# Kernel optimization log

Measured on AMD Instinct MI355X. Metric: run time of the kernel, lower is better.

## Reference

```python
import jax, jax.numpy as jnp
import numpy as np

N_P, N_A, N_S = 100000, 150000, 1000
D_IN, N_HID, N_OUT = 256, 256, 64
E_PA, E_PS = 800000, 100000
HOP = 3


def spmm(row, col, val, h, n_rows):
    # sparse A (edge list) @ dense h : gather source rows, scale, scatter-add to dest rows
    return jax.ops.segment_sum(val[:, None] * h[col], row, num_segments=n_rows)


def setup_inputs() -> dict:
    key = jax.random.key(0)
    ks = jax.random.split(key, 30)
    inp = {}
    inp['x_P'] = jax.random.normal(ks[0], (N_P, D_IN), jnp.float32)
    inp['x_A'] = jax.random.normal(ks[1], (N_A, D_IN), jnp.float32)
    inp['x_S'] = jax.random.normal(ks[2], (N_S, D_IN), jnp.float32)
    inp['pa_row'] = jax.random.randint(ks[3], (E_PA,), 0, N_P, jnp.int32)
    inp['pa_col'] = jax.random.randint(ks[4], (E_PA,), 0, N_A, jnp.int32)
    inp['pa_val'] = jax.random.uniform(ks[5], (E_PA,), jnp.float32)
    inp['ps_row'] = jax.random.randint(ks[6], (E_PS,), 0, N_P, jnp.int32)
    inp['ps_col'] = jax.random.randint(ks[7], (E_PS,), 0, N_S, jnp.int32)
    inp['ps_val'] = jax.random.uniform(ks[8], (E_PS,), jnp.float32)
    inp['ap_row'] = jax.random.randint(ks[9], (E_PA,), 0, N_A, jnp.int32)
    inp['ap_col'] = jax.random.randint(ks[10], (E_PA,), 0, N_P, jnp.int32)
    inp['ap_val'] = jax.random.uniform(ks[11], (E_PA,), jnp.float32)
    inp['sp_row'] = jax.random.randint(ks[12], (E_PS,), 0, N_S, jnp.int32)
    inp['sp_col'] = jax.random.randint(ks[13], (E_PS,), 0, N_P, jnp.int32)
    inp['sp_val'] = jax.random.uniform(ks[14], (E_PS,), jnp.float32)
    inp['diag_PA'] = jax.random.uniform(ks[15], (N_P, 1), jnp.float32)
    inp['diag_PS'] = jax.random.uniform(ks[16], (N_P, 1), jnp.float32)
    inp['diag_AP'] = jax.random.uniform(ks[17], (N_A, 1), jnp.float32)
    inp['diag_SP'] = jax.random.uniform(ks[18], (N_S, 1), jnp.float32)
    s1 = 0.05
    inp['W1_P'] = jax.random.normal(ks[19], (D_IN, N_HID), jnp.float32) * s1
    inp['b1_P'] = jnp.zeros((N_HID,), jnp.float32)
    inp['W1_A'] = jax.random.normal(ks[20], (D_IN, N_HID), jnp.float32) * s1
    inp['b1_A'] = jnp.zeros((N_HID,), jnp.float32)
    inp['W1_S'] = jax.random.normal(ks[21], (D_IN, N_HID), jnp.float32) * s1
    inp['b1_S'] = jnp.zeros((N_HID,), jnp.float32)
    inp['W2'] = jax.random.normal(ks[22], (N_HID, N_OUT), jnp.float32) * s1
    inp['b2'] = jnp.zeros((N_OUT,), jnp.float32)
    return inp


def reference(x_P, x_A, x_S,
              pa_row, pa_col, pa_val,
              ps_row, ps_col, ps_val,
              ap_row, ap_col, ap_val,
              sp_row, sp_col, sp_val,
              diag_PA, diag_PS, diag_AP, diag_SP,
              W1_P, b1_P, W1_A, b1_A, W1_S, b1_S, W2, b2):
    # input projections (dropout is identity in eval mode)
    xP = jax.nn.relu(x_P @ W1_P + b1_P)
    xA = jax.nn.relu(x_A @ W1_A + b1_A)
    xS = jax.nn.relu(x_S @ W1_S + b1_S)
    hP, hA, hS = xP, xA, xS
    # hop loop; node types updated sequentially (P, A, S) as in the torch dict loop
    for _ in range(HOP):
        hP = 0.5 * ((spmm(pa_row, pa_col, pa_val, hA, N_P) + diag_PA * xP)
                    + (spmm(ps_row, ps_col, ps_val, hS, N_P) + diag_PS * xP))
        hA = spmm(ap_row, ap_col, ap_val, hP, N_A) + diag_AP * xA
        hS = spmm(sp_row, sp_col, sp_val, hP, N_S) + diag_SP * xS
    # target_node_type = 'P'
    return hP @ W2 + b2
```

## Files before the change

kernel.cpp:

```cpp
#include <hip/hip_runtime.h>
#include <hip/hip_bf16.h>


typedef __attribute__((ext_vector_type(8))) short bf16x8;
typedef __attribute__((ext_vector_type(4))) float f32x4;

__device__ inline unsigned short f2bf(float f) {
    unsigned u = __builtin_bit_cast(unsigned, f);
    u += 0x7FFFu + ((u >> 16) & 1u);
    return (unsigned short)(u >> 16);
}
__device__ inline float bflo(unsigned u) { return __builtin_bit_cast(float, u << 16); }
__device__ inline float bfhi(unsigned u) { return __builtin_bit_cast(float, u & 0xffff0000u); }

__device__ inline void bar_sync() {
    __builtin_amdgcn_sched_barrier(0);
    asm volatile("s_waitcnt lgkmcnt(0)" ::: "memory");
    __builtin_amdgcn_s_barrier();
    __builtin_amdgcn_sched_barrier(0);
}

__global__ void k_prep_count(const float* __restrict__ W1P, const float* __restrict__ W1A,
                             const float* __restrict__ W1S, const float* __restrict__ W2f,
                             unsigned short* __restrict__ out,
                             const int* __restrict__ pa, const int* __restrict__ ps,
                             const int* __restrict__ ap, const int* __restrict__ sp,
                             int* __restrict__ cnt, int nP, int nA, int ePA, int ePS) {
    int i = blockIdx.x * 256 + threadIdx.x;
    if (i < 3 * 65536) {
        int m = i >> 16;
        int r = i & 65535;
        int j = r & 7, l = (r >> 3) & 63, kk = (r >> 9) & 7, nt = (r >> 12) & 15;
        int col = nt * 16 + (l & 15);
        int k = kk * 32 + ((l >> 4) << 3) + j;
        const float* s = (m == 0) ? W1P : (m == 1) ? W1A : W1S;
        out[i] = f2bf(s[k * 256 + col]);
        return;
    } else if (i < 3 * 65536 + 16384) {
        int r = i - 3 * 65536;
        int j = r & 7, l = (r >> 3) & 63, kk = (r >> 9) & 7, nt = (r >> 12) & 3;
        int col = nt * 16 + (l & 15);
        int k = kk * 32 + ((l >> 4) << 3) + j;
        out[i] = f2bf(W2f[k * 64 + col]);
        return;
    }
    i -= 212992;
    int r, base;
    if (i < 0) return;
    if (i < ePA) { r = pa[i]; base = 0; }
    else if (i < ePA + ePS) { r = ps[i - ePA]; base = nP; }
    else if (i < 2 * ePA + ePS) { r = ap[i - ePA - ePS]; base = 2 * nP; }
    else if (i < 2 * ePA + 2 * ePS) { r = sp[i - 2 * ePA - ePS]; base = 2 * nP + nA; }
    else return;
    atomicAdd(&cnt[base + r], 1);
}

__global__ __launch_bounds__(256)
void k_proj_all(const float* __restrict__ xP, const float* __restrict__ xA,
                const float* __restrict__ xS, const unsigned short* __restrict__ Wpk,
                const float* __restrict__ b1P, const float* __restrict__ b1A,
                const float* __restrict__ b1S,
                unsigned short* __restrict__ yP, unsigned short* __restrict__ yA,
                unsigned short* __restrict__ yS, int nP, int nA, int nS) {
    __shared__ unsigned short xs[32 * 256];
    const int TP = (nP + 31) >> 5, TA = (nA + 31) >> 5, TS = (nS + 31) >> 5;
    const int TT = TP + TA + TS;
    const int tid = threadIdx.x, lane = tid & 63, w = tid >> 6;
    const int l15 = lane & 15, lhi = lane >> 4;
    const unsigned short* W2pk = Wpk + 3 * 65536;

    float4 xr[8];
    int t = blockIdx.x;
    if (t >= TT) return;

    {
        const float* x; int r0, nn;
        if (t < TP) { x = xP; r0 = t << 5; nn = nP; }
        else if (t < TP + TA) { x = xA; r0 = (t - TP) << 5; nn = nA; }
        else { x = xS; r0 = (t - TP - TA) << 5; nn = nS; }
        #pragma unroll
        for (int j = 0; j < 4; ++j) {
            int c = tid + j * 256;
            int row = c >> 5, col = (c & 31) << 3;
            int gr = r0 + row;
            float4 z = make_float4(0, 0, 0, 0);
            xr[2 * j] = z; xr[2 * j + 1] = z;
            if (gr < nn) {
                const float4* p = (const float4*)(x + (size_t)gr * 256 + col);
                xr[2 * j] = p[0]; xr[2 * j + 1] = p[1];
            }
        }
    }
    while (t < TT) {
        const unsigned short* W1; const float* b1; unsigned short* y; int r0, nn;
        if (t < TP) { r0 = t << 5; nn = nP; W1 = Wpk; b1 = b1P; y = yP; }
        else if (t < TP + TA) { r0 = (t - TP) << 5; nn = nA; W1 = Wpk + 65536; b1 = b1A; y = yA; }
        else { r0 = (t - TP - TA) << 5; nn = nS; W1 = Wpk + 2 * 65536; b1 = b1S; y = yS; }

        bar_sync();
        #pragma unroll
        for (int j = 0; j < 4; ++j) {
            int c = tid + j * 256;
            int row = c >> 5, col = (c & 31) << 3;
            float4 f0 = xr[2 * j], f1 = xr[2 * j + 1];
            bf16x8 v;
            v[0] = (short)f2bf(f0.x); v[1] = (short)f2bf(f0.y);
            v[2] = (short)f2bf(f0.z); v[3] = (short)f2bf(f0.w);
            v[4] = (short)f2bf(f1.x); v[5] = (short)f2bf(f1.y);
            v[6] = (short)f2bf(f1.z); v[7] = (short)f2bf(f1.w);
            int byte = row * 512 + ((col * 2) ^ ((row & 7) << 4));
            *(bf16x8*)((char*)xs + byte) = v;
        }
        int tn = t + gridDim.x;
        if (tn < TT) {
            const float* x2; int r02, n2;
            if (tn < TP) { x2 = xP; r02 = tn << 5; n2 = nP; }
            else if (tn < TP + TA) { x2 = xA; r02 = (tn - TP) << 5; n2 = nA; }
            else { x2 = xS; r02 = (tn - TP - TA) << 5; n2 = nS; }
            #pragma unroll
            for (int j = 0; j < 4; ++j) {
                int c = tid + j * 256;
                int row = c >> 5, col = (c & 31) << 3;
                int gr = r02 + row;
                float4 z = make_float4(0, 0, 0, 0), a0 = z, a1 = z;
                if (gr < n2) {
                    const float4* q = (const float4*)(x2 + (size_t)gr * 256 + col);
                    a0 = q[0]; a1 = q[1];
                }
                xr[2 * j] = a0; xr[2 * j + 1] = a1;
            }
        }
        bar_sync();

        f32x4 acc[2][4] = {};
        #pragma unroll
        for (int kk = 0; kk < 8; ++kk) {
            int k = kk * 32 + lhi * 8;
            bf16x8 a[2], b[4];
            #pragma unroll
            for (int m = 0; m < 2; ++m) {
                int row = m * 16 + l15;
                int byte = row * 512 + ((k * 2) ^ ((row & 7) << 4));
                a[m] = *(const bf16x8*)((const char*)xs + byte);
            }
            #pragma unroll
            for (int nq = 0; nq < 4; ++nq)
                b[nq] = *(const bf16x8*)(W1 + ((((w * 4 + nq) * 8 + kk) * 64 + lane) << 3));
            #pragma unroll
            for (int m = 0; m < 2; ++m)
                #pragma unroll
                for (int nq = 0; nq < 4; ++nq)
                    acc[m][nq] = __builtin_amdgcn_mfma_f32_16x16x32_bf16(a[m], b[nq], acc[m][nq], 0, 0, 0);
        }
        bar_sync();

        #pragma unroll
        for (int nq = 0; nq < 4; ++nq) {
            int col = w * 64 + nq * 16 + l15;
            float bias = b1[col];
            #pragma unroll
            for (int m = 0; m < 2; ++m)
                #pragma unroll
                for (int q = 0; q < 4; ++q) {
                    int row = m * 16 + lhi * 4 + q;
                    float vv = acc[m][nq][q] + bias;
                    vv = vv > 0.f ? vv : 0.f;
                    int byte = row * 512 + ((col * 2) ^ ((row & 7) << 4));
                    *(unsigned short*)((char*)xs + byte) = f2bf(vv);
                }
        }
        bar_sync();

        if (w < 2) {
            f32x4 acc2[4] = {};
            #pragma unroll
            for (int kk = 0; kk < 8; ++kk) {
                int k = kk * 32 + lhi * 8;
                int row = w * 16 + l15;
                int byte = row * 512 + ((k * 2) ^ ((row & 7) << 4));
                bf16x8 a = *(const bf16x8*)((const char*)xs + byte);
                #pragma unroll
                for (int nq = 0; nq < 4; ++nq) {
                    bf16x8 b = *(const bf16x8*)(W2pk + (((nq * 8 + kk) * 64 + lane) << 3));
                    acc2[nq] = __builtin_amdgcn_mfma_f32_16x16x32_bf16(a, b, acc2[nq], 0, 0, 0);
                }
            }
            #pragma unroll
            for (int nq = 0; nq < 4; ++nq)
                #pragma unroll
                for (int q = 0; q < 4; ++q) {
                    int row = w * 16 + lhi * 4 + q;
                    int gr = r0 + row;
                    if (gr < nn) y[(size_t)gr * 64 + (nq * 16 + l15)] = f2bf(acc2[nq][q]);
                }
        }
        t = tn;
    }
}

__global__ __launch_bounds__(256)
void k_scan1(const int* __restrict__ cnt, int* __restrict__ off,
             int* __restrict__ bsum, int n) {
    __shared__ int sh[256];
    int tid = threadIdx.x;
    int base = blockIdx.x * 1024 + tid * 4;
    int c[4];
    #pragma unroll
    for (int j = 0; j < 4; ++j) c[j] = (base + j < n) ? cnt[base + j] : 0;
    int s = c[0] + c[1] + c[2] + c[3];
    sh[tid] = s;
    __syncthreads();
    #pragma unroll
    for (int o = 1; o < 256; o <<= 1) {
        int v = (tid >= o) ? sh[tid - o] : 0;
        __syncthreads();
        sh[tid] += v;
        __syncthreads();
    }
    int run = sh[tid] - s;
    #pragma unroll
    for (int j = 0; j < 4; ++j) {
        if (base + j < n) off[base + j] = run;
        run += c[j];
    }
    if (tid == 255) bsum[blockIdx.x] = sh[255];
}

__global__ __launch_bounds__(256)
void k_scan2(int* __restrict__ bsum, int nb) {
    __shared__ int sh[256];
    int tid = threadIdx.x;
    int base = tid * 4;
    int v[4];
    #pragma unroll
    for (int j = 0; j < 4; ++j) v[j] = (base + j < nb) ? bsum[base + j] : 0;
    int s = v[0] + v[1] + v[2] + v[3];
    sh[tid] = s;
    __syncthreads();
    #pragma unroll
    for (int o = 1; o < 256; o <<= 1) {
        int x = (tid >= o) ? sh[tid - o] : 0;
        __syncthreads();
        sh[tid] += x;
        __syncthreads();
    }
    int run = sh[tid] - s;
    #pragma unroll
    for (int j = 0; j < 4; ++j) {
        if (base + j < nb) bsum[base + j] = run;
        run += v[j];
    }
}

__global__ void k_scan3(const int* __restrict__ off0, const int* __restrict__ bsum,
                        int* __restrict__ offPA, int* __restrict__ offPS,
                        int* __restrict__ offAP, int* __restrict__ offSP,
                        int* __restrict__ curPA, int* __restrict__ curPS,
                        int* __restrict__ curAP, int* __restrict__ curSP,
                        int nP, int nA, int nS, int ePA, int ePS) {
    int i = blockIdx.x * 256 + threadIdx.x;
    int NC = 2 * nP + nA + nS;
    if (i >= NC) return;
    int v = off0[i] + bsum[i >> 10];
    int g0, loc, ng, nE; int *og, *cg;
    if (i < nP)                { g0 = 0;           loc = i;                ng = nP; nE = ePA; og = offPA; cg = curPA; }
    else if (i < 2 * nP)       { g0 = nP;          loc = i - nP;           ng = nP; nE = ePS; og = offPS; cg = curPS; }
    else if (i < 2 * nP + nA)  { g0 = 2 * nP;      loc = i - 2 * nP;       ng = nA; nE = ePA; og = offAP; cg = curAP; }
    else                       { g0 = 2 * nP + nA; loc = i - 2 * nP - nA;  ng = nS; nE = ePS; og = offSP; cg = curSP; }
    int basev = off0[g0] + bsum[g0 >> 10];
    int rel = v - basev;
    og[loc] = rel; cg[loc] = rel;
    if (loc == 0) og[ng] = nE;
}

__global__ void k_scatter_all(const int* __restrict__ pa_r, const int* __restrict__ pa_c, const float* __restrict__ pa_v,
                              const int* __restrict__ ps_r, const int* __restrict__ ps_c, const float* __restrict__ ps_v,
                              const int* __restrict__ ap_r, const int* __restrict__ ap_c, const float* __restrict__ ap_v,
                              const int* __restrict__ sp_r, const int* __restrict__ sp_c, const float* __restrict__ sp_v,
                              int* __restrict__ curPA, int* __restrict__ curPS,
                              int* __restrict__ curAP, int* __restrict__ curSP,
                              int2* __restrict__ entPA, int2* __restrict__ entPS,
                              int2* __restrict__ entAP, int2* __restrict__ entSP,
                              int ePA, int ePS) {
    int i = blockIdx.x * 256 + threadIdx.x;
    const int *r, *c; const float* v; int* cur; int2* ent; int e;
    if (i < ePA) { e = i; r = pa_r; c = pa_c; v = pa_v; cur = curPA; ent = entPA; }
    else if (i < ePA + ePS) { e = i - ePA; r = ps_r; c = ps_c; v = ps_v; cur = curPS; ent = entPS; }
    else if (i < 2 * ePA + ePS) { e = i - ePA - ePS; r = ap_r; c = ap_c; v = ap_v; cur = curAP; ent = entAP; }
    else if (i < 2 * ePA + 2 * ePS) { e = i - 2 * ePA - ePS; r = sp_r; c = sp_c; v = sp_v; cur = curSP; ent = entSP; }
    else return;
    int rr = r[e];
    int pp = atomicAdd(&cur[rr], 1);
    ent[pp] = make_int2(c[e], __float_as_int(v[e]));
}

__device__ inline void fma8(float acc[8], float w, uint4 g) {
    acc[0] = fmaf(w, bflo(g.x), acc[0]); acc[1] = fmaf(w, bfhi(g.x), acc[1]);
    acc[2] = fmaf(w, bflo(g.y), acc[2]); acc[3] = fmaf(w, bfhi(g.y), acc[3]);
    acc[4] = fmaf(w, bflo(g.z), acc[4]); acc[5] = fmaf(w, bfhi(g.z), acc[5]);
    acc[6] = fmaf(w, bflo(g.w), acc[6]); acc[7] = fmaf(w, bfhi(g.w), acc[7]);
}

__device__ inline void oct_pipe(const int2* __restrict__ ent, int s, int t,
                                const unsigned short* __restrict__ src,
                                int sub, int chunk, float acc[8]) {
    if (s >= t) return;
    int i0 = s + sub;
    int c0 = i0 < t ? i0 : t - 1;
    int2 Ea = ent[c0];
    float wa = i0 < t ? __int_as_float(Ea.y) : 0.f;
    uint4 ga = ((const uint4*)(src + ((size_t)(unsigned)Ea.x << 6)))[chunk];
    for (int e = s; ; ) {
        int en = e + 8;
        if (en < t) {
            int i1 = en + sub;
            int c1 = i1 < t ? i1 : t - 1;
            int2 Eb = ent[c1];
            float wb = i1 < t ? __int_as_float(Eb.y) : 0.f;
            uint4 gb = ((const uint4*)(src + ((size_t)(unsigned)Eb.x << 6)))[chunk];
            fma8(acc, wa, ga);
            wa = wb; ga = gb; e = en;
        } else {
            fma8(acc, wa, ga);
            break;
        }
    }
}

__device__ inline void red8(float acc[8]) {
    #pragma unroll
    for (int j = 0; j < 8; ++j) {
        acc[j] += __shfl_xor(acc[j], 8, 64);
        acc[j] += __shfl_xor(acc[j], 16, 64);
        acc[j] += __shfl_xor(acc[j], 32, 64);
    }
}

__device__ inline uint4 pack8(const float acc[8]) {
    uint4 o;
    o.x = (unsigned)f2bf(acc[0]) | ((unsigned)f2bf(acc[1]) << 16);
    o.y = (unsigned)f2bf(acc[2]) | ((unsigned)f2bf(acc[3]) << 16);
    o.z = (unsigned)f2bf(acc[4]) | ((unsigned)f2bf(acc[5]) << 16);
    o.w = (unsigned)f2bf(acc[6]) | ((unsigned)f2bf(acc[7]) << 16);
    return o;
}

__global__ __launch_bounds__(256)
void k_rowAS(unsigned short* __restrict__ hA, const unsigned short* __restrict__ yA,
             const float* __restrict__ dAP, const int* __restrict__ offAP,
             const int2* __restrict__ entAP,
             unsigned short* __restrict__ hS, const unsigned short* __restrict__ yS,
             const float* __restrict__ dSP, const int* __restrict__ offSP,
             const int2* __restrict__ entSP,
             const unsigned short* __restrict__ srcP, int nA, int nS) {
    int r = (blockIdx.x * 256 + threadIdx.x) >> 6;
    int lane = threadIdx.x & 63;
    int sub = lane >> 3, chunk = lane & 7;
    const int* off; const int2* ent; const unsigned short* y;
    const float* dg; unsigned short* dst;
    if (r < nA) { off = offAP; ent = entAP; y = yA; dg = dAP; dst = hA; }
    else if ((r -= nA) < nS) { off = offSP; ent = entSP; y = yS; dg = dSP; dst = hS; }
    else return;
    float acc[8] = {};
    int s = off[r], t = off[r + 1];
    float d = dg[r];
    uint4 gy = ((const uint4*)(y + (size_t)r * 64))[chunk];
    oct_pipe(ent, s, t, srcP, sub, chunk, acc);
    red8(acc);
    if (sub == 0) {
        acc[0] += d * bflo(gy.x); acc[1] += d * bfhi(gy.x);
        acc[2] += d * bflo(gy.y); acc[3] += d * bfhi(gy.y);
        acc[4] += d * bflo(gy.z); acc[5] += d * bfhi(gy.z);
        acc[6] += d * bflo(gy.w); acc[7] += d * bfhi(gy.w);
        ((uint4*)(dst + (size_t)r * 64))[chunk] = pack8(acc);
    }
}

template<int FINAL>
__global__ __launch_bounds__(256)
void k_row2(unsigned short* __restrict__ dst, float* __restrict__ dstf,
            const unsigned short* __restrict__ yP,
            const float* __restrict__ dA, const float* __restrict__ dB,
            const int* __restrict__ offA, const int2* __restrict__ entA,
            const unsigned short* __restrict__ srcA,
            const int* __restrict__ offB, const int2* __restrict__ entB,
            const unsigned short* __restrict__ srcB,
            const float* __restrict__ b2, int n) {
    int r = (blockIdx.x * 256 + threadIdx.x) >> 6;
    int lane = threadIdx.x & 63;
    int sub = lane >> 3, chunk = lane & 7;
    if (r >= n) return;
    float acc[8] = {};
    int sA = offA[r], tA = offA[r + 1];
    int sB = offB[r], tB = offB[r + 1];
    float d = dA[r] + dB[r];
    uint4 gy = ((const uint4*)(yP + (size_t)r * 64))[chunk];

    bool hasB = sB < tB;
    float wB = 0.f; uint4 gB;
    if (hasB) {
        int iB = sB + sub;
        int cB = iB < tB ? iB : tB - 1;
        int2 EB = entB[cB];
        wB = iB < tB ? __int_as_float(EB.y) : 0.f;
        gB = ((const uint4*)(srcB + ((size_t)(unsigned)EB.x << 6)))[chunk];
    }
    oct_pipe(entA, sA, tA, srcA, sub, chunk, acc);
    if (hasB) {
        fma8(acc, wB, gB);
        if (sB + 8 < tB) oct_pipe(entB, sB + 8, tB, srcB, sub, chunk, acc);
    }
    red8(acc);
    if (sub == 0) {
        acc[0] = 0.5f * (acc[0] + d * bflo(gy.x)); acc[1] = 0.5f * (acc[1] + d * bfhi(gy.x));
        acc[2] = 0.5f * (acc[2] + d * bflo(gy.y)); acc[3] = 0.5f * (acc[3] + d * bfhi(gy.y));
        acc[4] = 0.5f * (acc[4] + d * bflo(gy.z)); acc[5] = 0.5f * (acc[5] + d * bfhi(gy.z));
        acc[6] = 0.5f * (acc[6] + d * bflo(gy.w)); acc[7] = 0.5f * (acc[7] + d * bfhi(gy.w));
        if (FINAL) {
            float4 b0 = ((const float4*)b2)[chunk * 2];
            float4 b1v = ((const float4*)b2)[chunk * 2 + 1];
            float4 o0 = make_float4(acc[0] + b0.x, acc[1] + b0.y, acc[2] + b0.z, acc[3] + b0.w);
            float4 o1 = make_float4(acc[4] + b1v.x, acc[5] + b1v.y, acc[6] + b1v.z, acc[7] + b1v.w);
            ((float4*)(dstf + (size_t)r * 64))[chunk * 2] = o0;
            ((float4*)(dstf + (size_t)r * 64))[chunk * 2 + 1] = o1;
        } else {
            ((uint4*)(dst + (size_t)r * 64))[chunk] = pack8(acc);
        }
    }
}

extern "C" void kernel_launch(void* const* d_in, const int* in_sizes, int n_in,
                              void* d_out, int out_size, void* d_ws, size_t ws_size,
                              hipStream_t stream) {
    const float* x_P = (const float*)d_in[0];
    const float* x_A = (const float*)d_in[1];
    const float* x_S = (const float*)d_in[2];
    const int* pa_row = (const int*)d_in[3];
    const int* pa_col = (const int*)d_in[4];
    const float* pa_val = (const float*)d_in[5];
    const int* ps_row = (const int*)d_in[6];
    const int* ps_col = (const int*)d_in[7];
    const float* ps_val = (const float*)d_in[8];
    const int* ap_row = (const int*)d_in[9];
    const int* ap_col = (const int*)d_in[10];
    const float* ap_val = (const float*)d_in[11];
    const int* sp_row = (const int*)d_in[12];
    const int* sp_col = (const int*)d_in[13];
    const float* sp_val = (const float*)d_in[14];
    const float* diag_PA = (const float*)d_in[15];
    const float* diag_PS = (const float*)d_in[16];
    const float* diag_AP = (const float*)d_in[17];
    const float* diag_SP = (const float*)d_in[18];
    const float* W1_P = (const float*)d_in[19];
    const float* b1_P = (const float*)d_in[20];
    const float* W1_A = (const float*)d_in[21];
    const float* b1_A = (const float*)d_in[22];
    const float* W1_S = (const float*)d_in[23];
    const float* b1_S = (const float*)d_in[24];
    const float* W2  = (const float*)d_in[25];
    const float* b2  = (const float*)d_in[26];

    const int nP = in_sizes[15], nA = in_sizes[17], nS = in_sizes[18];
    const int ePA = in_sizes[3], ePS = in_sizes[6];
    const int NC = 2 * nP + nA + nS;

    char* base = (char*)d_ws;
    size_t cur = 0;
    auto alloc = [&](size_t bytes) -> char* {
        cur = (cur + 255) & ~(size_t)255;
        char* p = base + cur;
        cur += bytes;
        return p;
    };
    unsigned short* yP = (unsigned short*)alloc((size_t)nP * 64 * 2);
    unsigned short* yA = (unsigned short*)alloc((size_t)nA * 64 * 2);
    unsigned short* yS = (unsigned short*)alloc((size_t)nS * 64 * 2);
    unsigned short* hP = (unsigned short*)alloc((size_t)nP * 64 * 2);
    unsigned short* hA = (unsigned short*)alloc((size_t)nA * 64 * 2);
    unsigned short* hS = (unsigned short*)alloc((size_t)nS * 64 * 2);
    unsigned short* Wpk = (unsigned short*)alloc(212992 * 2);
    int* cnt  = (int*)alloc((size_t)NC * 4);
    int* off0 = (int*)alloc((size_t)NC * 4);
    int* offPA = (int*)alloc((size_t)(nP + 1) * 4);
    int* offPS = (int*)alloc((size_t)(nP + 1) * 4);
    int* offAP = (int*)alloc((size_t)(nA + 1) * 4);
    int* offSP = (int*)alloc((size_t)(nS + 1) * 4);
    int* curPA = (int*)alloc((size_t)nP * 4);
    int* curPS = (int*)alloc((size_t)nP * 4);
    int* curAP = (int*)alloc((size_t)nA * 4);
    int* curSP = (int*)alloc((size_t)nS * 4);
    int2* entPA = (int2*)alloc((size_t)ePA * 8);
    int2* entPS = (int2*)alloc((size_t)ePS * 8);
    int2* entAP = (int2*)alloc((size_t)ePA * 8);
    int2* entSP = (int2*)alloc((size_t)ePS * 8);
    int* bsum = (int*)alloc(1024 * 4);
    (void)ws_size;

    hipMemsetAsync(cnt, 0, (size_t)NC * 4, stream);
    const int eTot = 2 * (ePA + ePS);
    k_prep_count<<<(212992 + eTot + 255) / 256, 256, 0, stream>>>(
        W1_P, W1_A, W1_S, W2, Wpk,
        pa_row, ps_row, ap_row, sp_row, cnt, nP, nA, ePA, ePS);
    const int nb = (NC + 1023) / 1024;
    k_scan1<<<nb, 256, 0, stream>>>(cnt, off0, bsum, NC);
    k_scan2<<<1, 256, 0, stream>>>(bsum, nb);
    k_scan3<<<(NC + 255) / 256, 256, 0, stream>>>(off0, bsum, offPA, offPS, offAP, offSP,
                                                  curPA, curPS, curAP, curSP,
                                                  nP, nA, nS, ePA, ePS);
    k_scatter_all<<<(eTot + 255) / 256, 256, 0, stream>>>(
        pa_row, pa_col, pa_val, ps_row, ps_col, ps_val,
        ap_row, ap_col, ap_val, sp_row, sp_col, sp_val,
        curPA, curPS, curAP, curSP, entPA, entPS, entAP, entSP, ePA, ePS);

    k_proj_all<<<1024, 256, 0, stream>>>(x_P, x_A, x_S, Wpk, b1_P, b1_A, b1_S,
                                         yP, yA, yS, nP, nA, nS);

    const int gbP = (nP + 3) / 4, gbAS = (nA + nS + 3) / 4;
    k_row2<0><<<gbP, 256, 0, stream>>>(hP, nullptr, yP, diag_PA, diag_PS,
                                       offPA, entPA, yA, offPS, entPS, yS, b2, nP);
    k_rowAS<<<gbAS, 256, 0, stream>>>(hA, yA, diag_AP, offAP, entAP,
                                      hS, yS, diag_SP, offSP, entSP, hP, nA, nS);
    k_row2<0><<<gbP, 256, 0, stream>>>(hP, nullptr, yP, diag_PA, diag_PS,
                                       offPA, entPA, hA, offPS, entPS, hS, b2, nP);
    k_rowAS<<<gbAS, 256, 0, stream>>>(hA, yA, diag_AP, offAP, entAP,
                                      hS, yS, diag_SP, offSP, entSP, hP, nA, nS);
    k_row2<1><<<gbP, 256, 0, stream>>>(nullptr, (float*)d_out, yP, diag_PA, diag_PS,
                                       offPA, entPA, hA, offPS, entPS, hS, b2, nP);
}
```

Measured before the change: 582.0 us.

## Partition CSR scatter atomics by destination-row range per XCD

The edge scatter kernel now launches 8x as many blocks. Block index mod 8 picks an XCD, and each block handles only edges whose destination row falls in that XCD's eighth of the row range. The goal is to keep the atomic counters and entry writes local to one XCD's L2 and avoid cross-die coherence traffic. Edge arrays are read with nontemporal loads. The cost is reading every row index eight times and launching many more mostly-idle threads.

```diff
diff --git a/kernel.cpp b/kernel.cpp
--- a/kernel.cpp
+++ b/kernel.cpp
@@ -273,25 +273,31 @@
     if (loc == 0) og[ng] = nE;
 }
 
-__global__ void k_scatter_all(const int* __restrict__ pa_r, const int* __restrict__ pa_c, const float* __restrict__ pa_v,
-                              const int* __restrict__ ps_r, const int* __restrict__ ps_c, const float* __restrict__ ps_v,
-                              const int* __restrict__ ap_r, const int* __restrict__ ap_c, const float* __restrict__ ap_v,
-                              const int* __restrict__ sp_r, const int* __restrict__ sp_c, const float* __restrict__ sp_v,
-                              int* __restrict__ curPA, int* __restrict__ curPS,
-                              int* __restrict__ curAP, int* __restrict__ curSP,
-                              int2* __restrict__ entPA, int2* __restrict__ entPS,
-                              int2* __restrict__ entAP, int2* __restrict__ entSP,
-                              int ePA, int ePS) {
-    int i = blockIdx.x * 256 + threadIdx.x;
-    const int *r, *c; const float* v; int* cur; int2* ent; int e;
-    if (i < ePA) { e = i; r = pa_r; c = pa_c; v = pa_v; cur = curPA; ent = entPA; }
-    else if (i < ePA + ePS) { e = i - ePA; r = ps_r; c = ps_c; v = ps_v; cur = curPS; ent = entPS; }
-    else if (i < 2 * ePA + ePS) { e = i - ePA - ePS; r = ap_r; c = ap_c; v = ap_v; cur = curAP; ent = entAP; }
-    else if (i < 2 * ePA + 2 * ePS) { e = i - 2 * ePA - ePS; r = sp_r; c = sp_c; v = sp_v; cur = curSP; ent = entSP; }
+__global__ __launch_bounds__(256)
+void k_scatter_all(const int* __restrict__ pa_r, const int* __restrict__ pa_c, const float* __restrict__ pa_v,
+                   const int* __restrict__ ps_r, const int* __restrict__ ps_c, const float* __restrict__ ps_v,
+                   const int* __restrict__ ap_r, const int* __restrict__ ap_c, const float* __restrict__ ap_v,
+                   const int* __restrict__ sp_r, const int* __restrict__ sp_c, const float* __restrict__ sp_v,
+                   int* __restrict__ curPA, int* __restrict__ curPS,
+                   int* __restrict__ curAP, int* __restrict__ curSP,
+                   int2* __restrict__ entPA, int2* __restrict__ entPS,
+                   int2* __restrict__ entAP, int2* __restrict__ entSP,
+                   int nP, int nA, int nS, int ePA, int ePS) {
+    int xcd = blockIdx.x & 7;
+    int i = (blockIdx.x >> 3) * 256 + threadIdx.x;
+    const int *r, *c; const float* v; int* cur; int2* ent; int e, n;
+    if (i < ePA) { e = i; r = pa_r; c = pa_c; v = pa_v; cur = curPA; ent = entPA; n = nP; }
+    else if (i < ePA + ePS) { e = i - ePA; r = ps_r; c = ps_c; v = ps_v; cur = curPS; ent = entPS; n = nP; }
+    else if (i < 2 * ePA + ePS) { e = i - ePA - ePS; r = ap_r; c = ap_c; v = ap_v; cur = curAP; ent = entAP; n = nA; }
+    else if (i < 2 * ePA + 2 * ePS) { e = i - 2 * ePA - ePS; r = sp_r; c = sp_c; v = sp_v; cur = curSP; ent = entSP; n = nS; }
     else return;
-    int rr = r[e];
+    int rr = __builtin_nontemporal_load(r + e);
+    int r8 = rr * 8;
+    if (r8 < xcd * n || r8 >= (xcd + 1) * n) return;
+    int cc = __builtin_nontemporal_load(c + e);
+    float vv = __builtin_nontemporal_load(v + e);
     int pp = atomicAdd(&cur[rr], 1);
-    ent[pp] = make_int2(c[e], __float_as_int(v[e]));
+    ent[pp] = make_int2(cc, __float_as_int(vv));
 }
 
 __device__ inline void fma8(float acc[8], float w, uint4 g) {
@@ -507,10 +513,12 @@
     k_scan3<<<(NC + 255) / 256, 256, 0, stream>>>(off0, bsum, offPA, offPS, offAP, offSP,
                                                   curPA, curPS, curAP, curSP,
                                                   nP, nA, nS, ePA, ePS);
-    k_scatter_all<<<(eTot + 255) / 256, 256, 0, stream>>>(
+    const int SCB = (eTot + 255) / 256;
+    k_scatter_all<<<8 * SCB, 256, 0, stream>>>(
         pa_row, pa_col, pa_val, ps_row, ps_col, ps_val,
         ap_row, ap_col, ap_val, sp_row, sp_col, sp_val,
-        curPA, curPS, curAP, curSP, entPA, entPS, entAP, entSP, ePA, ePS);
+        curPA, curPS, curAP, curSP, entPA, entPS, entAP, entSP,
+        nP, nA, nS, ePA, ePS);
 
     k_proj_all<<<1024, 256, 0, stream>>>(x_P, x_A, x_S, Wpk, b1_P, b1_A, b1_S,
                                          yP, yA, yS, nP, nA, nS);
```

New measurement: 558.2 us, median of 2. -4.1%, faster.
